# Performance work log

Measured on AMD Instinct MI355X. Metric: run time of the kernel, lower is better.

## Reference

```python
import jax, jax.numpy as jnp
import numpy as np

B, T, C, H = 2, 2048, 1024, 16
D = C // H  # head dim = 64
NEG_MIN = jnp.finfo(jnp.float32).min


def setup_inputs() -> dict:
    key = jax.random.key(0)
    ks = jax.random.split(key, 5)
    std = 0.02
    return {
        "x": jax.random.normal(ks[0], (B, T, C), dtype=jnp.float32),
        "Wq": std * jax.random.normal(ks[1], (C, C), dtype=jnp.float32),
        "bq": jnp.zeros((C,), dtype=jnp.float32),
        "Wk": std * jax.random.normal(ks[2], (C, C), dtype=jnp.float32),
        "bk": jnp.zeros((C,), dtype=jnp.float32),
        "Wv": std * jax.random.normal(ks[3], (C, C), dtype=jnp.float32),
        "bv": jnp.zeros((C,), dtype=jnp.float32),
        "Wo": (std / np.sqrt(24.0)) * jax.random.normal(ks[4], (C, C), dtype=jnp.float32),
        "bo": jnp.zeros((C,), dtype=jnp.float32),
    }


def reference(x, Wq, bq, Wk, bk, Wv, bv, Wo, bo):
    # QKV projections -> (B, H, T, D)
    def proj(W, b):
        return (x @ W + b).reshape(B, T, H, D).transpose(0, 2, 1, 3)

    q = proj(Wq, bq)
    k = proj(Wk, bk)
    v = proj(Wv, bv)

    # full scores (B, H, T, T), causal mask, softmax
    attn = jnp.einsum("bhqd,bhkd->bhqk", q, k) / jnp.sqrt(jnp.float32(D))
    mask = jnp.tril(jnp.ones((T, T), dtype=bool))[None, None]
    attn = jnp.where(mask, attn, NEG_MIN)
    scores = jax.nn.softmax(attn, axis=-1)

    out = jnp.einsum("bhqk,bhkd->bhqd", scores, v)
    out = out.transpose(0, 2, 1, 3).reshape(B, T, C)
    return out @ Wo + bo
```

## Files before the change

### kernel.cpp

```cpp
#include <hip/hip_runtime.h>
#include <stdint.h>
#include <stddef.h>


#define B_SZ 2
#define T_SZ 2048
#define C_SZ 1024
#define H_SZ 16
#define D_SZ 64
#define M_SZ (B_SZ * T_SZ)
#define BHTD (B_SZ * H_SZ * T_SZ * D_SZ)
#define CC (C_SZ * C_SZ)

typedef __attribute__((ext_vector_type(8))) __bf16 bf16x8;
typedef __attribute__((ext_vector_type(4))) float f32x4;
typedef __attribute__((ext_vector_type(16))) float f32x16;

__device__ __forceinline__ unsigned short f2bf(float f) {
    union { float f; unsigned u; } v; v.f = f;
    v.u += 0x7fffu + ((v.u >> 16) & 1u);
    return (unsigned short)(v.u >> 16);
}

__device__ __forceinline__ unsigned pkbf(float lo, float hi_) {
    union { unsigned u; __bf16 h[2]; } r;
    r.h[0] = (__bf16)lo; r.h[1] = (__bf16)hi_;
    return r.u;
}

__device__ __forceinline__ void load_lds16(const unsigned short* g, unsigned short* l) {
    __builtin_amdgcn_global_load_lds(
        (const __attribute__((address_space(1))) void*)g,
        (__attribute__((address_space(3))) void*)l, 16, 0, 0);
}


__global__ void cvt_x_kernel(const float4* __restrict__ in, ushort4* __restrict__ out, int n4) {
    int stride = gridDim.x * blockDim.x;
    for (int i = blockIdx.x * blockDim.x + threadIdx.x; i < n4; i += stride) {
        float4 v = in[i];
        ushort4 o;
        o.x = f2bf(v.x); o.y = f2bf(v.y); o.z = f2bf(v.z); o.w = f2bf(v.w);
        out[i] = o;
    }
}

__global__ __launch_bounds__(256) void transpose_cvt_kernel(
    const float* __restrict__ W0, const float* __restrict__ W1,
    const float* __restrict__ W2, const float* __restrict__ W3,
    unsigned short* __restrict__ T0, unsigned short* __restrict__ T1,
    unsigned short* __restrict__ T2, unsigned short* __restrict__ T3)
{
    __shared__ float tile[32][33];
    const float* W; unsigned short* Wt;
    switch (blockIdx.z) {
        case 0: W = W0; Wt = T0; break;
        case 1: W = W1; Wt = T1; break;
        case 2: W = W2; Wt = T2; break;
        default: W = W3; Wt = T3; break;
    }
    const int tx = threadIdx.x, ty = threadIdx.y;
    const int n0 = blockIdx.x * 32, k0 = blockIdx.y * 32;
    #pragma unroll
    for (int i = 0; i < 4; i++)
        tile[ty + i * 8][tx] = W[(size_t)(k0 + ty + i * 8) * C_SZ + n0 + tx];
    __syncthreads();
    #pragma unroll
    for (int i = 0; i < 4; i++)
        Wt[(size_t)(n0 + ty + i * 8) * C_SZ + k0 + tx] = f2bf(tile[tx][ty + i * 8]);
}

__global__ __launch_bounds__(256) void vt_kernel(
    const unsigned short* __restrict__ V, unsigned short* __restrict__ Vt)
{
    __shared__ unsigned short tile[32][33];
    const int bh = blockIdx.z;
    const int t0 = blockIdx.x * 32, d0 = blockIdx.y * 32;
    const unsigned short* src = V + (size_t)bh * T_SZ * D_SZ;
    unsigned short* dst = Vt + (size_t)bh * T_SZ * D_SZ;
    const int tx = threadIdx.x, ty = threadIdx.y;
    #pragma unroll
    for (int i = 0; i < 4; i++)
        tile[ty + i * 8][tx] = src[(size_t)(t0 + ty + i * 8) * D_SZ + d0 + tx];
    __syncthreads();
    #pragma unroll
    for (int i = 0; i < 4; i++)
        dst[(size_t)(d0 + ty + i * 8) * T_SZ + t0 + tx] = tile[tx][ty + i * 8];
}


__device__ __forceinline__ void gemm_tile_core(
    const unsigned short* __restrict__ A,
    const unsigned short* __restrict__ Bt,
    unsigned short* As, unsigned short* Bs,
    int m0, int n0, f32x4 acc[4][4])
{
    const int tid = threadIdx.x;
    const int lane = tid & 63;
    const int w = tid >> 6;
    const int l15 = lane & 15, lg = lane >> 4;
    const int wr = (w >> 1) * 64, wc = (w & 1) * 64;

    const unsigned short* Ag0 = A + (size_t)(m0 + (tid >> 2)) * C_SZ + (tid & 3) * 8;
    const unsigned short* Ag1 = Ag0 + (size_t)64 * C_SZ;
    const unsigned short* Bg0 = Bt + (size_t)(n0 + (tid >> 2)) * C_SZ + (tid & 3) * 8;
    const unsigned short* Bg1 = Bg0 + (size_t)64 * C_SZ;
    unsigned short* As0 = As + w * 512;
    unsigned short* As1 = As + 2048 + w * 512;
    unsigned short* Bs0 = Bs + w * 512;
    unsigned short* Bs1 = Bs + 2048 + w * 512;

    for (int k0 = 0; k0 < C_SZ; k0 += 32) {
        load_lds16(Ag0 + k0, As0);
        load_lds16(Ag1 + k0, As1);
        load_lds16(Bg0 + k0, Bs0);
        load_lds16(Bg1 + k0, Bs1);
        __syncthreads();
        bf16x8 af[4], bfv[4];
        const bf16x8* Ap = (const bf16x8*)As;
        const bf16x8* Bp = (const bf16x8*)Bs;
        #pragma unroll
        for (int m = 0; m < 4; m++) af[m] = Ap[(wr + m * 16 + l15) * 4 + lg];
        #pragma unroll
        for (int n = 0; n < 4; n++) bfv[n] = Bp[(wc + n * 16 + l15) * 4 + lg];
        #pragma unroll
        for (int m = 0; m < 4; m++)
            #pragma unroll
            for (int n = 0; n < 4; n++)
                acc[m][n] = __builtin_amdgcn_mfma_f32_16x16x32_bf16(af[m], bfv[n], acc[m][n], 0, 0, 0);
        __syncthreads();
    }
}

__global__ __launch_bounds__(256) void gemm_qkv_kernel(
    const unsigned short* __restrict__ A,
    const unsigned short* __restrict__ WtBase,
    const float* __restrict__ bq, const float* __restrict__ bk, const float* __restrict__ bv,
    unsigned short* __restrict__ QKV, unsigned short* __restrict__ Vtmp)
{
    __shared__ unsigned short As[4096], Bs[4096];
    const int z = blockIdx.x >> 3;
    const unsigned short* Bt = WtBase + (size_t)z * CC;
    const float* bias = (z == 0) ? bq : (z == 1) ? bk : bv;
    const float scale = (z == 0) ? 0.18033688011112042f : 1.0f;
    unsigned short* Out = (z == 2) ? Vtmp : QKV + (size_t)z * BHTD;

    f32x4 acc[4][4];
    f32x4 zero4 = {0.f, 0.f, 0.f, 0.f};
    #pragma unroll
    for (int m = 0; m < 4; m++)
        #pragma unroll
        for (int n = 0; n < 4; n++) acc[m][n] = zero4;

    const int m0 = blockIdx.y * 128, n0 = (blockIdx.x & 7) * 128;
    gemm_tile_core(A, Bt, As, Bs, m0, n0, acc);

    const int lane = threadIdx.x & 63;
    const int w = threadIdx.x >> 6;
    const int l15 = lane & 15, lg = lane >> 4;
    const int wr = (w >> 1) * 64, wc = (w & 1) * 64;
    #pragma unroll
    for (int n = 0; n < 4; n++) {
        const int col = n0 + wc + n * 16 + l15;
        const float bias_v = bias[col];
        const int h = col >> 6, d = col & 63;
        #pragma unroll
        for (int m = 0; m < 4; m++) {
            #pragma unroll
            for (int j = 0; j < 4; j++) {
                const int row = m0 + wr + m * 16 + lg * 4 + j;
                const int b = row >> 11, t = row & (T_SZ - 1);
                Out[(((size_t)(b * H_SZ + h)) * T_SZ + t) * D_SZ + d] =
                    f2bf((acc[m][n][j] + bias_v) * scale);
            }
        }
    }
}

__global__ __launch_bounds__(256) void gemm_out_kernel(
    const unsigned short* __restrict__ A,
    const unsigned short* __restrict__ Bt,
    const float* __restrict__ bo,
    float* __restrict__ Out)
{
    __shared__ unsigned short As[2048], Bs[4096];
    const int tid = threadIdx.x;
    const int lane = tid & 63;
    const int w = tid >> 6;
    const int l15 = lane & 15, lg = lane >> 4;
    const int wc = w * 32;
    const int m0 = blockIdx.y * 64, n0 = blockIdx.x * 128;

    const unsigned short* Ag  = A + (size_t)(m0 + (tid >> 2)) * C_SZ + (tid & 3) * 8;
    const unsigned short* Bg0 = Bt + (size_t)(n0 + (tid >> 2)) * C_SZ + (tid & 3) * 8;
    const unsigned short* Bg1 = Bg0 + (size_t)64 * C_SZ;
    unsigned short* As0 = As + w * 512;
    unsigned short* Bs0 = Bs + w * 512;
    unsigned short* Bs1 = Bs + 2048 + w * 512;

    f32x4 acc[4][2];
    f32x4 zero4 = {0.f, 0.f, 0.f, 0.f};
    #pragma unroll
    for (int m = 0; m < 4; m++)
        #pragma unroll
        for (int n = 0; n < 2; n++) acc[m][n] = zero4;

    for (int k0 = 0; k0 < C_SZ; k0 += 32) {
        load_lds16(Ag + k0, As0);
        load_lds16(Bg0 + k0, Bs0);
        load_lds16(Bg1 + k0, Bs1);
        __syncthreads();
        bf16x8 af[4], bfv[2];
        const bf16x8* Ap = (const bf16x8*)As;
        const bf16x8* Bp = (const bf16x8*)Bs;
        #pragma unroll
        for (int m = 0; m < 4; m++) af[m] = Ap[(m * 16 + l15) * 4 + lg];
        #pragma unroll
        for (int n = 0; n < 2; n++) bfv[n] = Bp[(wc + n * 16 + l15) * 4 + lg];
        #pragma unroll
        for (int m = 0; m < 4; m++)
            #pragma unroll
            for (int n = 0; n < 2; n++)
                acc[m][n] = __builtin_amdgcn_mfma_f32_16x16x32_bf16(af[m], bfv[n], acc[m][n], 0, 0, 0);
        __syncthreads();
    }

    #pragma unroll
    for (int n = 0; n < 2; n++) {
        const int col = n0 + wc + n * 16 + l15;
        const float bias_v = bo[col];
        #pragma unroll
        for (int m = 0; m < 4; m++) {
            #pragma unroll
            for (int j = 0; j < 4; j++) {
                const int row = m0 + m * 16 + lg * 4 + j;
                Out[(size_t)row * C_SZ + col] = acc[m][n][j] + bias_v;
            }
        }
    }
}

__global__ __launch_bounds__(256) void attn_fwd_kernel(
    const unsigned short* __restrict__ Q,
    const unsigned short* __restrict__ K,
    const unsigned short* __restrict__ Vt,
    unsigned short* __restrict__ O)
{
    const int idx = blockIdx.x;
    const int qt = (idx < 256) ? (15 - (idx >> 5)) : ((idx - 256) >> 5);
    const int bh = idx & 31;
    const int w = threadIdx.x >> 6;
    const int lane = threadIdx.x & 63;
    const int l31 = lane & 31, hi = lane >> 5;
    const int qw = qt * 128 + 32 * w;

    const unsigned short* Qh = Q + (size_t)bh * T_SZ * D_SZ;
    const unsigned short* Kh = K + (size_t)bh * T_SZ * D_SZ;
    const unsigned short* Vh = Vt + (size_t)bh * T_SZ * D_SZ;

    __shared__ __align__(16) unsigned short smem[16384];

    const int c0 = w * 64 + lane;
    const int row0 = c0 >> 3;
    const int sw0 = (c0 & 7) ^ (row0 & 7);
    const int koff0 = row0 * 64 + sw0 * 8;
    const int voff0 = row0 * T_SZ + sw0 * 8;
    const int ldsb0 = w * 512;

    bf16x8 qf[4];
    #pragma unroll
    for (int j = 0; j < 4; j++)
        qf[j] = *(const bf16x8*)&Qh[(size_t)(qw + l31) * D_SZ + j * 16 + 8 * hi];

    f32x16 acc[2];
    #pragma unroll
    for (int r = 0; r < 16; r++) { acc[0][r] = 0.f; acc[1][r] = 0.f; }
    float mrun = -3.0e38f, lrun = 0.f;

    const int tlast = (qw + 31) >> 6;
    const int ntb = 2 * qt + 2;
    const int qrow = qw + l31;
    const int swl = l31 & 7;

    load_lds16(Kh + koff0, smem + ldsb0);
    load_lds16(Kh + koff0 + 2048, smem + 2048 + ldsb0);
    load_lds16(Vh + voff0, smem + 4096 + ldsb0);
    load_lds16(Vh + voff0 + 32 * T_SZ, smem + 6144 + ldsb0);

    for (int tt = 0; tt < ntb; ++tt) {
        if (tt + 1 < ntb) {
            unsigned short* Bd = smem + ((tt + 1) & 1) * 8192;
            const unsigned short* Kt = Kh + (size_t)(tt + 1) * 64 * D_SZ;
            const unsigned short* Vtt = Vh + (tt + 1) * 64;
            load_lds16(Kt + koff0, Bd + ldsb0);
            load_lds16(Kt + koff0 + 2048, Bd + 2048 + ldsb0);
            load_lds16(Vtt + voff0, Bd + 4096 + ldsb0);
            load_lds16(Vtt + voff0 + 32 * T_SZ, Bd + 6144 + ldsb0);
            asm volatile("s_waitcnt vmcnt(4)" ::: "memory");
        } else {
            asm volatile("s_waitcnt vmcnt(0)" ::: "memory");
        }
        __builtin_amdgcn_s_barrier();

        if (tt <= tlast) {
            const unsigned short* Ks = smem + (tt & 1) * 8192;
            const unsigned short* Vs = Ks + 4096;
            const int k0 = tt * 64;

            f32x16 s[2];
            #pragma unroll
            for (int kb = 0; kb < 2; ++kb) {
                bf16x8 kf[4];
                #pragma unroll
                for (int j = 0; j < 4; ++j) {
                    const int ch = (j * 2 + hi) ^ swl;
                    kf[j] = *(const bf16x8*)&Ks[(kb * 32 + l31) * 64 + ch * 8];
                }
                f32x16 sc;
                #pragma unroll
                for (int r = 0; r < 16; r++) sc[r] = 0.f;
                #pragma unroll
                for (int j = 0; j < 4; ++j)
                    sc = __builtin_amdgcn_mfma_f32_32x32x16_bf16(kf[j], qf[j], sc, 0, 0, 0);
                s[kb] = sc;
            }

            if (k0 + 63 > qw) {
                #pragma unroll
                for (int kb = 0; kb < 2; ++kb)
                    #pragma unroll
                    for (int r = 0; r < 16; ++r) {
                        const int kv = k0 + kb * 32 + (r & 3) + 8 * (r >> 2) + 4 * hi;
                        s[kb][r] = (kv > qrow) ? -3.0e38f : s[kb][r];
                    }
            }

            float t16[16];
            #pragma unroll
            for (int i = 0; i < 16; i++) t16[i] = fmaxf(s[0][i], s[1][i]);
            #pragma unroll
            for (int st = 8; st >= 1; st >>= 1)
                #pragma unroll
                for (int i = 0; i < st; i++) t16[i] = fmaxf(t16[i], t16[i + st]);
            const float pm = fmaxf(t16[0], __shfl_xor(t16[0], 32));

            if (!__all(pm <= mrun + 8.0f)) {
                const float mnew = fmaxf(mrun, pm);
                const float al = exp2f(mrun - mnew);
                lrun *= al;
                #pragma unroll
                for (int r = 0; r < 16; r++) { acc[0][r] *= al; acc[1][r] *= al; }
                mrun = mnew;
            }

            #pragma unroll
            for (int kb = 0; kb < 2; ++kb)
                #pragma unroll
                for (int r = 0; r < 16; r++) s[kb][r] = exp2f(s[kb][r] - mrun);
            float a16[16];
            #pragma unroll
            for (int i = 0; i < 16; i++) a16[i] = s[0][i] + s[1][i];
            #pragma unroll
            for (int st = 8; st >= 1; st >>= 1)
                #pragma unroll
                for (int i = 0; i < st; i++) a16[i] += a16[i + st];
            lrun += a16[0] + __shfl_xor(a16[0], 32);

            bf16x8 pf[2][2];
            #pragma unroll
            for (int kb = 0; kb < 2; ++kb) {
                #pragma unroll
                for (int ksl = 0; ksl < 2; ++ksl) {
                    unsigned a0 = pkbf(s[kb][8 * ksl + 0], s[kb][8 * ksl + 1]);
                    unsigned a1 = pkbf(s[kb][8 * ksl + 2], s[kb][8 * ksl + 3]);
                    unsigned b0 = pkbf(s[kb][8 * ksl + 4], s[kb][8 * ksl + 5]);
                    unsigned b1 = pkbf(s[kb][8 * ksl + 6], s[kb][8 * ksl + 7]);
                    asm volatile("v_permlane32_swap_b32 %0, %1" : "+v"(a0), "+v"(b0));
                    asm volatile("v_permlane32_swap_b32 %0, %1" : "+v"(a1), "+v"(b1));
                    union { unsigned u[4]; bf16x8 v; } fr;
                    fr.u[0] = a0; fr.u[1] = a1; fr.u[2] = b0; fr.u[3] = b1;
                    pf[kb][ksl] = fr.v;
                }
            }

            #pragma unroll
            for (int dt = 0; dt < 2; ++dt)
                #pragma unroll
                for (int kb = 0; kb < 2; ++kb)
                    #pragma unroll
                    for (int ksl = 0; ksl < 2; ++ksl) {
                        const int ks = kb * 2 + ksl;
                        const int ch = (ks * 2 + hi) ^ swl;
                        const bf16x8 vf = *(const bf16x8*)&Vs[(dt * 32 + l31) * 64 + ch * 8];
                        acc[dt] = __builtin_amdgcn_mfma_f32_32x32x16_bf16(vf, pf[kb][ksl], acc[dt], 0, 0, 0);
                    }
        }
        __builtin_amdgcn_s_barrier();
    }

    unsigned short* ot = smem + w * 2304;
    const float inv = 1.0f / lrun;
    #pragma unroll
    for (int g = 0; g < 4; g++) {
        ushort4 wa, wb;
        wa.x = f2bf(acc[0][4 * g + 0] * inv); wa.y = f2bf(acc[0][4 * g + 1] * inv);
        wa.z = f2bf(acc[0][4 * g + 2] * inv); wa.w = f2bf(acc[0][4 * g + 3] * inv);
        wb.x = f2bf(acc[1][4 * g + 0] * inv); wb.y = f2bf(acc[1][4 * g + 1] * inv);
        wb.z = f2bf(acc[1][4 * g + 2] * inv); wb.w = f2bf(acc[1][4 * g + 3] * inv);
        *(ushort4*)&ot[l31 * 72 + 8 * g + 4 * hi] = wa;
        *(ushort4*)&ot[l31 * 72 + 32 + 8 * g + 4 * hi] = wb;
    }
    const int b = bh >> 4, h = bh & 15;
    #pragma unroll
    for (int pss = 0; pss < 4; pss++) {
        const int q = pss * 8 + (lane >> 3);
        const uint4 val = *(const uint4*)&ot[q * 72 + (lane & 7) * 8];
        *(uint4*)&O[((size_t)(b * T_SZ + qw + q)) * C_SZ + h * D_SZ + (lane & 7) * 8] = val;
    }
}


extern "C" void kernel_launch(void* const* d_in, const int* in_sizes, int n_in,
                              void* d_out, int out_size, void* d_ws, size_t ws_size,
                              hipStream_t stream)
{
    const float* x  = (const float*)d_in[0];
    const float* Wq = (const float*)d_in[1];
    const float* bq = (const float*)d_in[2];
    const float* Wk = (const float*)d_in[3];
    const float* bk = (const float*)d_in[4];
    const float* Wv = (const float*)d_in[5];
    const float* bv = (const float*)d_in[6];
    const float* Wo = (const float*)d_in[7];
    const float* bo = (const float*)d_in[8];

    uint8_t* ws = (uint8_t*)d_ws;
    unsigned short* XB   = (unsigned short*)(ws);
    unsigned short* WT   = (unsigned short*)(ws + (8u  << 20));
    unsigned short* QKV  = (unsigned short*)(ws + (16u << 20));
    unsigned short* Vtmp = (unsigned short*)(ws + (40u << 20));

    cvt_x_kernel<<<2048, 256, 0, stream>>>((const float4*)x, (ushort4*)XB, M_SZ * C_SZ / 4);
    transpose_cvt_kernel<<<dim3(32, 32, 4), dim3(32, 8), 0, stream>>>(
        Wq, Wk, Wv, Wo, WT, WT + CC, WT + 2 * (size_t)CC, WT + 3 * (size_t)CC);
    gemm_qkv_kernel<<<dim3(24, 32), 256, 0, stream>>>(XB, WT, bq, bk, bv, QKV, Vtmp);
    vt_kernel<<<dim3(64, 2, 32), dim3(32, 8), 0, stream>>>(Vtmp, QKV + 2 * (size_t)BHTD);
    attn_fwd_kernel<<<512, 256, 0, stream>>>(
        QKV, QKV + BHTD, QKV + 2 * (size_t)BHTD, Vtmp);
    gemm_out_kernel<<<dim3(8, 64), 256, 0, stream>>>(Vtmp, WT + 3 * (size_t)CC, bo, (float*)d_out);
}
```

Baseline: 129.0 us.

## Give each attention wave private K/V staging with balanced causal query strips

Each wave now owns a private LDS region and streams its own 32-row K/V tiles, so the block-wide barriers inside the key loop go away. Query strips are assigned to waves in complementary pairs (2p, 63-2p, 2p+1, 62-2p), so every block carries about the same total causal work. The key tile shrinks from 64 to 32, so only the final tile needs masking. In exchange, K/V reuse across waves in a block is lost, which raises global and L2 traffic, and LDS use doubles to 64KB, which may cut occupancy.

```diff
diff --git a/kernel.cpp b/kernel.cpp
--- a/kernel.cpp
+++ b/kernel.cpp
@@ -246,26 +246,25 @@
     const unsigned short* __restrict__ Vt,
     unsigned short* __restrict__ O)
 {
-    const int idx = blockIdx.x;
-    const int qt = (idx < 256) ? (15 - (idx >> 5)) : ((idx - 256) >> 5);
-    const int bh = idx & 31;
+    const int i = blockIdx.x;
+    const int bh = i & 31;
+    const int p = i >> 5;
     const int w = threadIdx.x >> 6;
     const int lane = threadIdx.x & 63;
     const int l31 = lane & 31, hi = lane >> 5;
-    const int qw = qt * 128 + 32 * w;
+    const int qs = (w == 0) ? 2 * p : (w == 1) ? 63 - 2 * p
+                 : (w == 2) ? 2 * p + 1 : 62 - 2 * p;
+    const int qw = qs * 32;
 
     const unsigned short* Qh = Q + (size_t)bh * T_SZ * D_SZ;
     const unsigned short* Kh = K + (size_t)bh * T_SZ * D_SZ;
     const unsigned short* Vh = Vt + (size_t)bh * T_SZ * D_SZ;
 
-    __shared__ __align__(16) unsigned short smem[16384];
-
-    const int c0 = w * 64 + lane;
-    const int row0 = c0 >> 3;
-    const int sw0 = (c0 & 7) ^ (row0 & 7);
-    const int koff0 = row0 * 64 + sw0 * 8;
-    const int voff0 = row0 * T_SZ + sw0 * 8;
-    const int ldsb0 = w * 512;
+    __shared__ __align__(16) unsigned short smem[32768];
+    unsigned short* wb = smem + w * 8192;
+
+    const int koffb = (lane >> 3) * 64 + (((lane & 7) ^ (lane >> 3)) * 8);
+    const int voffb = (lane >> 2) * T_SZ + (((lane & 3) ^ ((lane >> 2) & 3)) * 8);
 
     bf16x8 qf[4];
     #pragma unroll
@@ -277,139 +276,122 @@
     for (int r = 0; r < 16; r++) { acc[0][r] = 0.f; acc[1][r] = 0.f; }
     float mrun = -3.0e38f, lrun = 0.f;
 
-    const int tlast = (qw + 31) >> 6;
-    const int ntb = 2 * qt + 2;
-    const int qrow = qw + l31;
-    const int swl = l31 & 7;
-
-    load_lds16(Kh + koff0, smem + ldsb0);
-    load_lds16(Kh + koff0 + 2048, smem + 2048 + ldsb0);
-    load_lds16(Vh + voff0, smem + 4096 + ldsb0);
-    load_lds16(Vh + voff0 + 32 * T_SZ, smem + 6144 + ldsb0);
+    const int ntb = qs + 1;
+    const int sw7 = l31 & 7, sw3 = l31 & 3;
+
+    #pragma unroll
+    for (int ii = 0; ii < 4; ii++)
+        load_lds16(Kh + ii * 512 + koffb, wb + ii * 512);
+    #pragma unroll
+    for (int ii = 0; ii < 4; ii++)
+        load_lds16(Vh + ii * 16 * T_SZ + voffb, wb + 2048 + ii * 512);
 
     for (int tt = 0; tt < ntb; ++tt) {
         if (tt + 1 < ntb) {
-            unsigned short* Bd = smem + ((tt + 1) & 1) * 8192;
-            const unsigned short* Kt = Kh + (size_t)(tt + 1) * 64 * D_SZ;
-            const unsigned short* Vtt = Vh + (tt + 1) * 64;
-            load_lds16(Kt + koff0, Bd + ldsb0);
-            load_lds16(Kt + koff0 + 2048, Bd + 2048 + ldsb0);
-            load_lds16(Vtt + voff0, Bd + 4096 + ldsb0);
-            load_lds16(Vtt + voff0 + 32 * T_SZ, Bd + 6144 + ldsb0);
-            asm volatile("s_waitcnt vmcnt(4)" ::: "memory");
+            unsigned short* bd = wb + ((tt + 1) & 1) * 4096;
+            const unsigned short* Kt = Kh + (size_t)(tt + 1) * 32 * D_SZ;
+            const unsigned short* Vn = Vh + (tt + 1) * 32;
+            #pragma unroll
+            for (int ii = 0; ii < 4; ii++)
+                load_lds16(Kt + ii * 512 + koffb, bd + ii * 512);
+            #pragma unroll
+            for (int ii = 0; ii < 4; ii++)
+                load_lds16(Vn + ii * 16 * T_SZ + voffb, bd + 2048 + ii * 512);
+            asm volatile("s_waitcnt vmcnt(8)" ::: "memory");
         } else {
             asm volatile("s_waitcnt vmcnt(0)" ::: "memory");
         }
-        __builtin_amdgcn_s_barrier();
-
-        if (tt <= tlast) {
-            const unsigned short* Ks = smem + (tt & 1) * 8192;
-            const unsigned short* Vs = Ks + 4096;
-            const int k0 = tt * 64;
-
-            f32x16 s[2];
-            #pragma unroll
-            for (int kb = 0; kb < 2; ++kb) {
-                bf16x8 kf[4];
-                #pragma unroll
-                for (int j = 0; j < 4; ++j) {
-                    const int ch = (j * 2 + hi) ^ swl;
-                    kf[j] = *(const bf16x8*)&Ks[(kb * 32 + l31) * 64 + ch * 8];
-                }
-                f32x16 sc;
-                #pragma unroll
-                for (int r = 0; r < 16; r++) sc[r] = 0.f;
-                #pragma unroll
-                for (int j = 0; j < 4; ++j)
-                    sc = __builtin_amdgcn_mfma_f32_32x32x16_bf16(kf[j], qf[j], sc, 0, 0, 0);
-                s[kb] = sc;
+
+        const unsigned short* Ks = wb + (tt & 1) * 4096;
+        const unsigned short* Vs = Ks + 2048;
+
+        bf16x8 kf[4];
+        #pragma unroll
+        for (int j = 0; j < 4; ++j) {
+            const int ch = (j * 2 + hi) ^ sw7;
+            kf[j] = *(const bf16x8*)&Ks[l31 * 64 + ch * 8];
+        }
+        f32x16 s;
+        #pragma unroll
+        for (int r = 0; r < 16; r++) s[r] = 0.f;
+        #pragma unroll
+        for (int j = 0; j < 4; ++j)
+            s = __builtin_amdgcn_mfma_f32_32x32x16_bf16(kf[j], qf[j], s, 0, 0, 0);
+
+        if (tt == ntb - 1) {
+            #pragma unroll
+            for (int r = 0; r < 16; r++) {
+                const int kvl = (r & 3) + 8 * (r >> 2) + 4 * hi;
+                s[r] = (kvl > l31) ? -3.0e38f : s[r];
             }
-
-            if (k0 + 63 > qw) {
-                #pragma unroll
-                for (int kb = 0; kb < 2; ++kb)
-                    #pragma unroll
-                    for (int r = 0; r < 16; ++r) {
-                        const int kv = k0 + kb * 32 + (r & 3) + 8 * (r >> 2) + 4 * hi;
-                        s[kb][r] = (kv > qrow) ? -3.0e38f : s[kb][r];
-                    }
+        }
+
+        float t8[8];
+        #pragma unroll
+        for (int k = 0; k < 8; k++) t8[k] = fmaxf(s[k], s[k + 8]);
+        #pragma unroll
+        for (int st = 4; st >= 1; st >>= 1)
+            #pragma unroll
+            for (int k = 0; k < st; k++) t8[k] = fmaxf(t8[k], t8[k + st]);
+        const float pm = fmaxf(t8[0], __shfl_xor(t8[0], 32));
+
+        if (!__all(pm <= mrun + 8.0f)) {
+            const float mnew = fmaxf(mrun, pm);
+            const float al = exp2f(mrun - mnew);
+            lrun *= al;
+            #pragma unroll
+            for (int r = 0; r < 16; r++) { acc[0][r] *= al; acc[1][r] *= al; }
+            mrun = mnew;
+        }
+
+        #pragma unroll
+        for (int r = 0; r < 16; r++) s[r] = exp2f(s[r] - mrun);
+        float a8[8];
+        #pragma unroll
+        for (int k = 0; k < 8; k++) a8[k] = s[k] + s[k + 8];
+        #pragma unroll
+        for (int st = 4; st >= 1; st >>= 1)
+            #pragma unroll
+            for (int k = 0; k < st; k++) a8[k] += a8[k + st];
+        lrun += a8[0] + __shfl_xor(a8[0], 32);
+
+        bf16x8 pf[2];
+        #pragma unroll
+        for (int ks = 0; ks < 2; ++ks) {
+            unsigned a0 = pkbf(s[8 * ks + 0], s[8 * ks + 1]);
+            unsigned a1 = pkbf(s[8 * ks + 2], s[8 * ks + 3]);
+            unsigned b0 = pkbf(s[8 * ks + 4], s[8 * ks + 5]);
+            unsigned b1 = pkbf(s[8 * ks + 6], s[8 * ks + 7]);
+            asm volatile("v_permlane32_swap_b32 %0, %1" : "+v"(a0), "+v"(b0));
+            asm volatile("v_permlane32_swap_b32 %0, %1" : "+v"(a1), "+v"(b1));
+            union { unsigned u[4]; bf16x8 v; } fr;
+            fr.u[0] = a0; fr.u[1] = a1; fr.u[2] = b0; fr.u[3] = b1;
+            pf[ks] = fr.v;
+        }
+
+        #pragma unroll
+        for (int dt = 0; dt < 2; ++dt)
+            #pragma unroll
+            for (int ks = 0; ks < 2; ++ks) {
+                const int ch = (ks * 2 + hi) ^ sw3;
+                const bf16x8 vf = *(const bf16x8*)&Vs[(dt * 32 + l31) * 32 + ch * 8];
+                acc[dt] = __builtin_amdgcn_mfma_f32_32x32x16_bf16(vf, pf[ks], acc[dt], 0, 0, 0);
             }
-
-            float t16[16];
-            #pragma unroll
-            for (int i = 0; i < 16; i++) t16[i] = fmaxf(s[0][i], s[1][i]);
-            #pragma unroll
-            for (int st = 8; st >= 1; st >>= 1)
-                #pragma unroll
-                for (int i = 0; i < st; i++) t16[i] = fmaxf(t16[i], t16[i + st]);
-            const float pm = fmaxf(t16[0], __shfl_xor(t16[0], 32));
-
-            if (!__all(pm <= mrun + 8.0f)) {
-                const float mnew = fmaxf(mrun, pm);
-                const float al = exp2f(mrun - mnew);
-                lrun *= al;
-                #pragma unroll
-                for (int r = 0; r < 16; r++) { acc[0][r] *= al; acc[1][r] *= al; }
-                mrun = mnew;
-            }
-
-            #pragma unroll
-            for (int kb = 0; kb < 2; ++kb)
-                #pragma unroll
-                for (int r = 0; r < 16; r++) s[kb][r] = exp2f(s[kb][r] - mrun);
-            float a16[16];
-            #pragma unroll
-            for (int i = 0; i < 16; i++) a16[i] = s[0][i] + s[1][i];
-            #pragma unroll
-            for (int st = 8; st >= 1; st >>= 1)
-                #pragma unroll
-                for (int i = 0; i < st; i++) a16[i] += a16[i + st];
-            lrun += a16[0] + __shfl_xor(a16[0], 32);
-
-            bf16x8 pf[2][2];
-            #pragma unroll
-            for (int kb = 0; kb < 2; ++kb) {
-                #pragma unroll
-                for (int ksl = 0; ksl < 2; ++ksl) {
-                    unsigned a0 = pkbf(s[kb][8 * ksl + 0], s[kb][8 * ksl + 1]);
-                    unsigned a1 = pkbf(s[kb][8 * ksl + 2], s[kb][8 * ksl + 3]);
-                    unsigned b0 = pkbf(s[kb][8 * ksl + 4], s[kb][8 * ksl + 5]);
-                    unsigned b1 = pkbf(s[kb][8 * ksl + 6], s[kb][8 * ksl + 7]);
-                    asm volatile("v_permlane32_swap_b32 %0, %1" : "+v"(a0), "+v"(b0));
-                    asm volatile("v_permlane32_swap_b32 %0, %1" : "+v"(a1), "+v"(b1));
-                    union { unsigned u[4]; bf16x8 v; } fr;
-                    fr.u[0] = a0; fr.u[1] = a1; fr.u[2] = b0; fr.u[3] = b1;
-                    pf[kb][ksl] = fr.v;
-                }
-            }
-
-            #pragma unroll
-            for (int dt = 0; dt < 2; ++dt)
-                #pragma unroll
-                for (int kb = 0; kb < 2; ++kb)
-                    #pragma unroll
-                    for (int ksl = 0; ksl < 2; ++ksl) {
-                        const int ks = kb * 2 + ksl;
-                        const int ch = (ks * 2 + hi) ^ swl;
-                        const bf16x8 vf = *(const bf16x8*)&Vs[(dt * 32 + l31) * 64 + ch * 8];
-                        acc[dt] = __builtin_amdgcn_mfma_f32_32x32x16_bf16(vf, pf[kb][ksl], acc[dt], 0, 0, 0);
-                    }
-        }
-        __builtin_amdgcn_s_barrier();
-    }
-
-    unsigned short* ot = smem + w * 2304;
+    }
+
+    unsigned short* ot = wb;
     const float inv = 1.0f / lrun;
     #pragma unroll
     for (int g = 0; g < 4; g++) {
-        ushort4 wa, wb;
+        ushort4 wa, wbv;
         wa.x = f2bf(acc[0][4 * g + 0] * inv); wa.y = f2bf(acc[0][4 * g + 1] * inv);
         wa.z = f2bf(acc[0][4 * g + 2] * inv); wa.w = f2bf(acc[0][4 * g + 3] * inv);
-        wb.x = f2bf(acc[1][4 * g + 0] * inv); wb.y = f2bf(acc[1][4 * g + 1] * inv);
-        wb.z = f2bf(acc[1][4 * g + 2] * inv); wb.w = f2bf(acc[1][4 * g + 3] * inv);
+        wbv.x = f2bf(acc[1][4 * g + 0] * inv); wbv.y = f2bf(acc[1][4 * g + 1] * inv);
+        wbv.z = f2bf(acc[1][4 * g + 2] * inv); wbv.w = f2bf(acc[1][4 * g + 3] * inv);
         *(ushort4*)&ot[l31 * 72 + 8 * g + 4 * hi] = wa;
-        *(ushort4*)&ot[l31 * 72 + 32 + 8 * g + 4 * hi] = wb;
-    }
+        *(ushort4*)&ot[l31 * 72 + 32 + 8 * g + 4 * hi] = wbv;
+    }
+    __syncthreads();
     const int b = bh >> 4, h = bh & 15;
     #pragma unroll
     for (int pss = 0; pss < 4; pss++) {
```

Result: slower. 143.1 us (+10.9%).

## Fuse V transpose into QKV GEMM epilogue and triple-buffer attention K/V loads

Applied to the files above, without the earlier changes.

The V projection tile is staged through shared memory in the QKV GEMM and written out directly in transposed [d][t] layout with vector stores. This removes the separate vt_kernel launch and its extra global round trip. The attention kernel moves from double to triple buffering of K/V tiles with adjusted waitcnt, trading more LDS for deeper prefetch. Row max and sum reductions are also rewritten as sequential chains.

```diff
diff --git a/kernel.cpp b/kernel.cpp
--- a/kernel.cpp
+++ b/kernel.cpp
@@ -68,24 +68,6 @@
     #pragma unroll
     for (int i = 0; i < 4; i++)
         Wt[(size_t)(n0 + ty + i * 8) * C_SZ + k0 + tx] = f2bf(tile[tx][ty + i * 8]);
-}
-
-__global__ __launch_bounds__(256) void vt_kernel(
-    const unsigned short* __restrict__ V, unsigned short* __restrict__ Vt)
-{
-    __shared__ unsigned short tile[32][33];
-    const int bh = blockIdx.z;
-    const int t0 = blockIdx.x * 32, d0 = blockIdx.y * 32;
-    const unsigned short* src = V + (size_t)bh * T_SZ * D_SZ;
-    unsigned short* dst = Vt + (size_t)bh * T_SZ * D_SZ;
-    const int tx = threadIdx.x, ty = threadIdx.y;
-    #pragma unroll
-    for (int i = 0; i < 4; i++)
-        tile[ty + i * 8][tx] = src[(size_t)(t0 + ty + i * 8) * D_SZ + d0 + tx];
-    __syncthreads();
-    #pragma unroll
-    for (int i = 0; i < 4; i++)
-        dst[(size_t)(d0 + ty + i * 8) * T_SZ + t0 + tx] = tile[tx][ty + i * 8];
 }
 
 
@@ -136,14 +118,16 @@
     const unsigned short* __restrict__ A,
     const unsigned short* __restrict__ WtBase,
     const float* __restrict__ bq, const float* __restrict__ bk, const float* __restrict__ bv,
-    unsigned short* __restrict__ QKV, unsigned short* __restrict__ Vtmp)
-{
-    __shared__ unsigned short As[4096], Bs[4096];
+    unsigned short* __restrict__ QKV)
+{
+    __shared__ __align__(16) unsigned short smem[17408];
+    unsigned short* As = smem;
+    unsigned short* Bs = smem + 4096;
     const int z = blockIdx.x >> 3;
     const unsigned short* Bt = WtBase + (size_t)z * CC;
     const float* bias = (z == 0) ? bq : (z == 1) ? bk : bv;
     const float scale = (z == 0) ? 0.18033688011112042f : 1.0f;
-    unsigned short* Out = (z == 2) ? Vtmp : QKV + (size_t)z * BHTD;
+    unsigned short* Out = QKV + (size_t)z * BHTD;
 
     f32x4 acc[4][4];
     f32x4 zero4 = {0.f, 0.f, 0.f, 0.f};
@@ -159,19 +143,45 @@
     const int w = threadIdx.x >> 6;
     const int l15 = lane & 15, lg = lane >> 4;
     const int wr = (w >> 1) * 64, wc = (w & 1) * 64;
-    #pragma unroll
-    for (int n = 0; n < 4; n++) {
-        const int col = n0 + wc + n * 16 + l15;
-        const float bias_v = bias[col];
-        const int h = col >> 6, d = col & 63;
-        #pragma unroll
-        for (int m = 0; m < 4; m++) {
-            #pragma unroll
-            for (int j = 0; j < 4; j++) {
-                const int row = m0 + wr + m * 16 + lg * 4 + j;
-                const int b = row >> 11, t = row & (T_SZ - 1);
-                Out[(((size_t)(b * H_SZ + h)) * T_SZ + t) * D_SZ + d] =
-                    f2bf((acc[m][n][j] + bias_v) * scale);
+    if (z == 2) {
+        unsigned short* ot = smem;
+        #pragma unroll
+        for (int n = 0; n < 4; n++) {
+            const int dp = wc + n * 16 + l15;
+            const float bias_v = bias[n0 + dp];
+            #pragma unroll
+            for (int m = 0; m < 4; m++)
+                #pragma unroll
+                for (int j = 0; j < 4; j++)
+                    ot[dp * 136 + wr + m * 16 + lg * 4 + j] = f2bf(acc[m][n][j] + bias_v);
+        }
+        __syncthreads();
+        const int b = m0 >> 11, t0 = m0 & (T_SZ - 1);
+        const int tid = threadIdx.x;
+        #pragma unroll
+        for (int k = 0; k < 8; k++) {
+            const int c = tid + k * 256;
+            const int dp = c >> 4, tc = c & 15;
+            const int col = n0 + dp;
+            const int h = col >> 6, d = col & 63;
+            const uint4 val = *(const uint4*)&ot[dp * 136 + tc * 8];
+            *(uint4*)&Out[(((size_t)(b * H_SZ + h)) * D_SZ + d) * T_SZ + t0 + tc * 8] = val;
+        }
+    } else {
+        #pragma unroll
+        for (int n = 0; n < 4; n++) {
+            const int col = n0 + wc + n * 16 + l15;
+            const float bias_v = bias[col];
+            const int h = col >> 6, d = col & 63;
+            #pragma unroll
+            for (int m = 0; m < 4; m++) {
+                #pragma unroll
+                for (int j = 0; j < 4; j++) {
+                    const int row = m0 + wr + m * 16 + lg * 4 + j;
+                    const int b = row >> 11, t = row & (T_SZ - 1);
+                    Out[(((size_t)(b * H_SZ + h)) * T_SZ + t) * D_SZ + d] =
+                        f2bf((acc[m][n][j] + bias_v) * scale);
+                }
             }
         }
     }
@@ -258,7 +268,7 @@
     const unsigned short* Kh = K + (size_t)bh * T_SZ * D_SZ;
     const unsigned short* Vh = Vt + (size_t)bh * T_SZ * D_SZ;
 
-    __shared__ __align__(16) unsigned short smem[16384];
+    __shared__ __align__(16) unsigned short smem[24576];
 
     const int c0 = w * 64 + lane;
     const int row0 = c0 >> 3;
@@ -282,20 +292,30 @@
     const int qrow = qw + l31;
     const int swl = l31 & 7;
 
-    load_lds16(Kh + koff0, smem + ldsb0);
-    load_lds16(Kh + koff0 + 2048, smem + 2048 + ldsb0);
-    load_lds16(Vh + voff0, smem + 4096 + ldsb0);
-    load_lds16(Vh + voff0 + 32 * T_SZ, smem + 6144 + ldsb0);
+    {
+        load_lds16(Kh + koff0, smem + ldsb0);
+        load_lds16(Kh + koff0 + 2048, smem + 2048 + ldsb0);
+        load_lds16(Vh + voff0, smem + 4096 + ldsb0);
+        load_lds16(Vh + voff0 + 32 * T_SZ, smem + 6144 + ldsb0);
+        const unsigned short* Kt = Kh + (size_t)64 * D_SZ;
+        const unsigned short* Vtt = Vh + 64;
+        load_lds16(Kt + koff0, smem + 8192 + ldsb0);
+        load_lds16(Kt + koff0 + 2048, smem + 10240 + ldsb0);
+        load_lds16(Vtt + voff0, smem + 12288 + ldsb0);
+        load_lds16(Vtt + voff0 + 32 * T_SZ, smem + 14336 + ldsb0);
+    }
 
     for (int tt = 0; tt < ntb; ++tt) {
-        if (tt + 1 < ntb) {
-            unsigned short* Bd = smem + ((tt + 1) & 1) * 8192;
-            const unsigned short* Kt = Kh + (size_t)(tt + 1) * 64 * D_SZ;
-            const unsigned short* Vtt = Vh + (tt + 1) * 64;
+        if (tt + 2 < ntb) {
+            unsigned short* Bd = smem + ((tt + 2) % 3) * 8192;
+            const unsigned short* Kt = Kh + (size_t)(tt + 2) * 64 * D_SZ;
+            const unsigned short* Vtt = Vh + (tt + 2) * 64;
             load_lds16(Kt + koff0, Bd + ldsb0);
             load_lds16(Kt + koff0 + 2048, Bd + 2048 + ldsb0);
             load_lds16(Vtt + voff0, Bd + 4096 + ldsb0);
             load_lds16(Vtt + voff0 + 32 * T_SZ, Bd + 6144 + ldsb0);
+            asm volatile("s_waitcnt vmcnt(8)" ::: "memory");
+        } else if (tt + 1 < ntb) {
             asm volatile("s_waitcnt vmcnt(4)" ::: "memory");
         } else {
             asm volatile("s_waitcnt vmcnt(0)" ::: "memory");
@@ -303,7 +323,7 @@
         __builtin_amdgcn_s_barrier();
 
         if (tt <= tlast) {
-            const unsigned short* Ks = smem + (tt & 1) * 8192;
+            const unsigned short* Ks = smem + (tt % 3) * 8192;
             const unsigned short* Vs = Ks + 4096;
             const int k0 = tt * 64;
 
@@ -335,14 +355,12 @@
                     }
             }
 
-            float t16[16];
-            #pragma unroll
-            for (int i = 0; i < 16; i++) t16[i] = fmaxf(s[0][i], s[1][i]);
-            #pragma unroll
-            for (int st = 8; st >= 1; st >>= 1)
-                #pragma unroll
-                for (int i = 0; i < st; i++) t16[i] = fmaxf(t16[i], t16[i + st]);
-            const float pm = fmaxf(t16[0], __shfl_xor(t16[0], 32));
+            float pm = s[0][0];
+            #pragma unroll
+            for (int r = 1; r < 16; r++) pm = fmaxf(pm, s[0][r]);
+            #pragma unroll
+            for (int r = 0; r < 16; r++) pm = fmaxf(pm, s[1][r]);
+            pm = fmaxf(pm, __shfl_xor(pm, 32));
 
             if (!__all(pm <= mrun + 8.0f)) {
                 const float mnew = fmaxf(mrun, pm);
@@ -353,18 +371,13 @@
                 mrun = mnew;
             }
 
+            float ps = 0.f;
             #pragma unroll
             for (int kb = 0; kb < 2; ++kb)
                 #pragma unroll
-                for (int r = 0; r < 16; r++) s[kb][r] = exp2f(s[kb][r] - mrun);
-            float a16[16];
-            #pragma unroll
-            for (int i = 0; i < 16; i++) a16[i] = s[0][i] + s[1][i];
-            #pragma unroll
-            for (int st = 8; st >= 1; st >>= 1)
-                #pragma unroll
-                for (int i = 0; i < st; i++) a16[i] += a16[i + st];
-            lrun += a16[0] + __shfl_xor(a16[0], 32);
+                for (int r = 0; r < 16; r++) { s[kb][r] = exp2f(s[kb][r] - mrun); ps += s[kb][r]; }
+            ps += __shfl_xor(ps, 32);
+            lrun += ps;
 
             bf16x8 pf[2][2];
             #pragma unroll
@@ -435,17 +448,16 @@
     const float* bo = (const float*)d_in[8];
 
     uint8_t* ws = (uint8_t*)d_ws;
-    unsigned short* XB   = (unsigned short*)(ws);
-    unsigned short* WT   = (unsigned short*)(ws + (8u  << 20));
-    unsigned short* QKV  = (unsigned short*)(ws + (16u << 20));
-    unsigned short* Vtmp = (unsigned short*)(ws + (40u << 20));
+    unsigned short* XB  = (unsigned short*)(ws);
+    unsigned short* WT  = (unsigned short*)(ws + (8u  << 20));
+    unsigned short* QKV = (unsigned short*)(ws + (16u << 20));
+    unsigned short* OB  = (unsigned short*)(ws + (40u << 20));
 
     cvt_x_kernel<<<2048, 256, 0, stream>>>((const float4*)x, (ushort4*)XB, M_SZ * C_SZ / 4);
     transpose_cvt_kernel<<<dim3(32, 32, 4), dim3(32, 8), 0, stream>>>(
         Wq, Wk, Wv, Wo, WT, WT + CC, WT + 2 * (size_t)CC, WT + 3 * (size_t)CC);
-    gemm_qkv_kernel<<<dim3(24, 32), 256, 0, stream>>>(XB, WT, bq, bk, bv, QKV, Vtmp);
-    vt_kernel<<<dim3(64, 2, 32), dim3(32, 8), 0, stream>>>(Vtmp, QKV + 2 * (size_t)BHTD);
+    gemm_qkv_kernel<<<dim3(24, 32), 256, 0, stream>>>(XB, WT, bq, bk, bv, QKV);
     attn_fwd_kernel<<<512, 256, 0, stream>>>(
-        QKV, QKV + BHTD, QKV + 2 * (size_t)BHTD, Vtmp);
-    gemm_out_kernel<<<dim3(8, 64), 256, 0, stream>>>(Vtmp, WT + 3 * (size_t)CC, bo, (float*)d_out);
-}
+        QKV, QKV + BHTD, QKV + 2 * (size_t)BHTD, OB);
+    gemm_out_kernel<<<dim3(8, 64), 256, 0, stream>>>(OB, WT + 3 * (size_t)CC, bo, (float*)d_out);
+}
```

Result: slower. 135.7 us (+5.1%).

## Triple-buffer K/V tiles in attention and use raw v_exp_f32

Applied to the files above, without the earlier changes.

Moves the flash-attention K/V shared-memory staging from double to triple buffering, prefetching two tiles ahead with matching vmcnt waits. The goal is to hide more global-load latency. It also swaps exp2f for an inline v_exp_f32 asm helper that skips the library's range handling, and rewrites the row max/sum reductions as four independent accumulator chains. In exchange, shared memory per block grows by half, which may lower occupancy, and the volatile asm with s_nop may limit how the compiler schedules these instructions.

```diff
diff --git a/kernel.cpp b/kernel.cpp
--- a/kernel.cpp
+++ b/kernel.cpp
@@ -26,6 +26,12 @@
     union { unsigned u; __bf16 h[2]; } r;
     r.h[0] = (__bf16)lo; r.h[1] = (__bf16)hi_;
     return r.u;
+}
+
+__device__ __forceinline__ float fexp2(float x) {
+    float r;
+    asm volatile("v_exp_f32 %0, %1\n\ts_nop 0" : "=v"(r) : "v"(x));
+    return r;
 }
 
 __device__ __forceinline__ void load_lds16(const unsigned short* g, unsigned short* l) {
@@ -258,7 +264,7 @@
     const unsigned short* Kh = K + (size_t)bh * T_SZ * D_SZ;
     const unsigned short* Vh = Vt + (size_t)bh * T_SZ * D_SZ;
 
-    __shared__ __align__(16) unsigned short smem[16384];
+    __shared__ __align__(16) unsigned short smem[24576];
 
     const int c0 = w * 64 + lane;
     const int row0 = c0 >> 3;
@@ -282,20 +288,30 @@
     const int qrow = qw + l31;
     const int swl = l31 & 7;
 
-    load_lds16(Kh + koff0, smem + ldsb0);
-    load_lds16(Kh + koff0 + 2048, smem + 2048 + ldsb0);
-    load_lds16(Vh + voff0, smem + 4096 + ldsb0);
-    load_lds16(Vh + voff0 + 32 * T_SZ, smem + 6144 + ldsb0);
+    {
+        load_lds16(Kh + koff0, smem + ldsb0);
+        load_lds16(Kh + koff0 + 2048, smem + 2048 + ldsb0);
+        load_lds16(Vh + voff0, smem + 4096 + ldsb0);
+        load_lds16(Vh + voff0 + 32 * T_SZ, smem + 6144 + ldsb0);
+        const unsigned short* Kt = Kh + (size_t)64 * D_SZ;
+        const unsigned short* Vtt = Vh + 64;
+        load_lds16(Kt + koff0, smem + 8192 + ldsb0);
+        load_lds16(Kt + koff0 + 2048, smem + 10240 + ldsb0);
+        load_lds16(Vtt + voff0, smem + 12288 + ldsb0);
+        load_lds16(Vtt + voff0 + 32 * T_SZ, smem + 14336 + ldsb0);
+    }
 
     for (int tt = 0; tt < ntb; ++tt) {
-        if (tt + 1 < ntb) {
-            unsigned short* Bd = smem + ((tt + 1) & 1) * 8192;
-            const unsigned short* Kt = Kh + (size_t)(tt + 1) * 64 * D_SZ;
-            const unsigned short* Vtt = Vh + (tt + 1) * 64;
+        if (tt + 2 < ntb) {
+            unsigned short* Bd = smem + ((tt + 2) % 3) * 8192;
+            const unsigned short* Kt = Kh + (size_t)(tt + 2) * 64 * D_SZ;
+            const unsigned short* Vtt = Vh + (tt + 2) * 64;
             load_lds16(Kt + koff0, Bd + ldsb0);
             load_lds16(Kt + koff0 + 2048, Bd + 2048 + ldsb0);
             load_lds16(Vtt + voff0, Bd + 4096 + ldsb0);
             load_lds16(Vtt + voff0 + 32 * T_SZ, Bd + 6144 + ldsb0);
+            asm volatile("s_waitcnt vmcnt(8)" ::: "memory");
+        } else if (tt + 1 < ntb) {
             asm volatile("s_waitcnt vmcnt(4)" ::: "memory");
         } else {
             asm volatile("s_waitcnt vmcnt(0)" ::: "memory");
@@ -303,7 +319,7 @@
         __builtin_amdgcn_s_barrier();
 
         if (tt <= tlast) {
-            const unsigned short* Ks = smem + (tt & 1) * 8192;
+            const unsigned short* Ks = smem + (tt % 3) * 8192;
             const unsigned short* Vs = Ks + 4096;
             const int k0 = tt * 64;
 
@@ -335,18 +351,21 @@
                     }
             }
 
-            float t16[16];
-            #pragma unroll
-            for (int i = 0; i < 16; i++) t16[i] = fmaxf(s[0][i], s[1][i]);
-            #pragma unroll
-            for (int st = 8; st >= 1; st >>= 1)
-                #pragma unroll
-                for (int i = 0; i < st; i++) t16[i] = fmaxf(t16[i], t16[i + st]);
-            const float pm = fmaxf(t16[0], __shfl_xor(t16[0], 32));
+            float pm0 = fmaxf(s[0][0], s[1][0]), pm1 = fmaxf(s[0][1], s[1][1]);
+            float pm2 = fmaxf(s[0][2], s[1][2]), pm3 = fmaxf(s[0][3], s[1][3]);
+            #pragma unroll
+            for (int r = 4; r < 16; r += 4) {
+                pm0 = fmaxf(pm0, fmaxf(s[0][r + 0], s[1][r + 0]));
+                pm1 = fmaxf(pm1, fmaxf(s[0][r + 1], s[1][r + 1]));
+                pm2 = fmaxf(pm2, fmaxf(s[0][r + 2], s[1][r + 2]));
+                pm3 = fmaxf(pm3, fmaxf(s[0][r + 3], s[1][r + 3]));
+            }
+            float pm = fmaxf(fmaxf(pm0, pm1), fmaxf(pm2, pm3));
+            pm = fmaxf(pm, __shfl_xor(pm, 32));
 
             if (!__all(pm <= mrun + 8.0f)) {
                 const float mnew = fmaxf(mrun, pm);
-                const float al = exp2f(mrun - mnew);
+                const float al = fexp2(mrun - mnew);
                 lrun *= al;
                 #pragma unroll
                 for (int r = 0; r < 16; r++) { acc[0][r] *= al; acc[1][r] *= al; }
@@ -356,15 +375,19 @@
             #pragma unroll
             for (int kb = 0; kb < 2; ++kb)
                 #pragma unroll
-                for (int r = 0; r < 16; r++) s[kb][r] = exp2f(s[kb][r] - mrun);
-            float a16[16];
-            #pragma unroll
-            for (int i = 0; i < 16; i++) a16[i] = s[0][i] + s[1][i];
-            #pragma unroll
-            for (int st = 8; st >= 1; st >>= 1)
-                #pragma unroll
-                for (int i = 0; i < st; i++) a16[i] += a16[i + st];
-            lrun += a16[0] + __shfl_xor(a16[0], 32);
+                for (int r = 0; r < 16; r++) s[kb][r] = fexp2(s[kb][r] - mrun);
+            float ps0 = s[0][0] + s[1][0], ps1 = s[0][1] + s[1][1];
+            float ps2 = s[0][2] + s[1][2], ps3 = s[0][3] + s[1][3];
+            #pragma unroll
+            for (int r = 4; r < 16; r += 4) {
+                ps0 += s[0][r + 0] + s[1][r + 0];
+                ps1 += s[0][r + 1] + s[1][r + 1];
+                ps2 += s[0][r + 2] + s[1][r + 2];
+                ps3 += s[0][r + 3] + s[1][r + 3];
+            }
+            float ps = (ps0 + ps1) + (ps2 + ps3);
+            ps += __shfl_xor(ps, 32);
+            lrun += ps;
 
             bf16x8 pf[2][2];
             #pragma unroll
```

Result: faster. 121.4 us (-5.9%).
